# Kernel tuning notes

Measured on AMD Instinct MI355X. Metric: run time of the kernel, lower is better.

## Reference

```python
import jax, jax.numpy as jnp
import numpy as np

GROUP_SIZE = 64
SCALING = 32.0 / 16.0  # lora_alpha / r


def setup_inputs() -> dict:
    key = jax.random.key(0)
    k = jax.random.split(key, 7)
    B, S, I, O, R = 4, 2048, 4096, 4096, 16
    G = I // GROUP_SIZE
    x = jax.random.normal(k[0], (B, S, I), dtype=jnp.float32)
    W_q = jax.random.randint(k[1], (O, I), 0, 16, dtype=jnp.int32)
    scale = jax.random.uniform(k[2], (O, G), dtype=jnp.float32) * 0.01 + 1e-4
    zero = jax.random.uniform(k[3], (O, G), dtype=jnp.float32) * 8.0
    lora_A = jax.random.normal(k[4], (I, R), dtype=jnp.float32) * 0.02
    lora_B = jax.random.normal(k[5], (R, O), dtype=jnp.float32) * 0.02
    bias = jax.random.normal(k[6], (O,), dtype=jnp.float32) * 0.01
    return {"x": x, "W_q": W_q, "scale": scale, "zero": zero,
            "lora_A": lora_A, "lora_B": lora_B, "bias": bias}


def reference(x, W_q, scale, zero, lora_A, lora_B, bias):
    O, I = W_q.shape
    G = I // GROUP_SIZE
    # HQQ-style group-wise affine dequant: W = (W_q - zero) * scale  -> [O, I]
    Wg = W_q.reshape(O, G, GROUP_SIZE).astype(scale.dtype)
    W = ((Wg - zero[:, :, None]) * scale[:, :, None]).reshape(O, I)
    # base quantized linear: out = x @ W^T
    out = jnp.einsum('bsi,oi->bso', x, W)
    # LoRA low-rank update (dropout is Identity for p=0)
    out = out + (x @ lora_A @ lora_B) * SCALING
    # bias add
    out = out + bias
    return out
```

## Files before the change

### kernel.cpp

```cpp
#include <hip/hip_runtime.h>
#include <hip/hip_bf16.h>
#include <stdint.h>

#define M_DIM 8192
#define N_DIM 4096
#define K_DIM 4096

typedef __attribute__((ext_vector_type(8))) __bf16 bf16x8;
typedef __attribute__((ext_vector_type(4))) float f32x4;

__device__ inline unsigned short f2bf(float f) {
  unsigned u = __builtin_bit_cast(unsigned, f);
  u += 0x7FFF + ((u >> 16) & 1);
  return (unsigned short)(u >> 16);
}

__device__ inline void async_copy16(const void* g, void* l) {
  __builtin_amdgcn_global_load_lds(
      (const __attribute__((address_space(1))) unsigned int*)g,
      (__attribute__((address_space(3))) unsigned int*)l, 16, 0, 0);
}

__global__ __launch_bounds__(256) void cvt_x_kernel(const float* __restrict__ x,
                                                    unsigned short* __restrict__ xb,
                                                    int n4) {
  int i = blockIdx.x * 256 + threadIdx.x;
  int stride = gridDim.x * 256;
  for (; i < n4; i += stride) {
    float4 v = reinterpret_cast<const float4*>(x)[i];
    ushort4 o;
    o.x = f2bf(v.x); o.y = f2bf(v.y); o.z = f2bf(v.z); o.w = f2bf(v.w);
    reinterpret_cast<ushort4*>(xb)[i] = o;
  }
}

__global__ __launch_bounds__(256) void build_weff_kernel(
    const int* __restrict__ Wq, const float* __restrict__ scale,
    const float* __restrict__ zero, const float* __restrict__ A,
    const float* __restrict__ Bm, unsigned short* __restrict__ Weff) {
  __shared__ float sA[64 * 17];
  __shared__ float sB[16 * 64];
  int bo = blockIdx.x >> 6;
  int bi = blockIdx.x & 63;
  int o0 = bo * 64, i0 = bi * 64;
  int t = threadIdx.x;
  for (int j = t; j < 1024; j += 256) sA[(j >> 4) * 17 + (j & 15)] = A[i0 * 16 + j];
  for (int j = t; j < 1024; j += 256) sB[j] = Bm[(j >> 6) * N_DIM + o0 + (j & 63)];
  __syncthreads();
  for (int e = 0; e < 16; ++e) {
    int idx = e * 256 + t;
    int oo = idx >> 6, ii = idx & 63;
    int o = o0 + oo;
    float sc = scale[o * 64 + bi];
    float zp = zero[o * 64 + bi];
    float w = ((float)Wq[(size_t)o * K_DIM + i0 + ii] - zp) * sc;
    float acc = 0.f;
#pragma unroll
    for (int r = 0; r < 16; ++r) acc += sA[ii * 17 + r] * sB[r * 64 + oo];
    w += 2.0f * acc;
    Weff[(size_t)o * K_DIM + i0 + ii] = f2bf(w);
  }
}

#define BAR() __builtin_amdgcn_s_barrier()
#define SB()  __builtin_amdgcn_sched_barrier(0)
#define WAIT_LGKM() do { asm volatile("s_waitcnt lgkmcnt(0)" ::: "memory"); SB(); } while (0)
#define WAIT_VM4()  do { asm volatile("s_waitcnt vmcnt(4)" ::: "memory"); } while (0)

__device__ __forceinline__ bf16x8 lds_frag(const unsigned short* region, int row, int c) {
  return *reinterpret_cast<const bf16x8*>(region + row * 64 + ((c ^ (row & 7)) << 3));
}

__device__ __forceinline__ void readA(const unsigned short* reg, int mh, int lc, int lr,
                                      bf16x8 a[4][2]) {
#pragma unroll
  for (int m = 0; m < 4; ++m) {
    int row = mh * 64 + m * 16 + lc;
#pragma unroll
    for (int kk = 0; kk < 2; ++kk) a[m][kk] = lds_frag(reg, row, kk * 4 + lr);
  }
}

__device__ __forceinline__ void readB(const unsigned short* reg, int nh, int rB, int lc, int lr,
                                      bf16x8 b[2][2]) {
#pragma unroll
  for (int n = 0; n < 2; ++n) {
    int row = rB + (nh * 2 + n) * 16 + lc;
#pragma unroll
    for (int kk = 0; kk < 2; ++kk) b[n][kk] = lds_frag(reg, row, kk * 4 + lr);
  }
}

__device__ __forceinline__ void mfma_quad(const bf16x8 a[4][2], const bf16x8 b[2][2],
                                          f32x4 acc[8][4], int mh, int nh) {
  __builtin_amdgcn_s_setprio(1);
#pragma unroll
  for (int m = 0; m < 4; ++m)
#pragma unroll
    for (int n = 0; n < 2; ++n)
#pragma unroll
      for (int kk = 0; kk < 2; ++kk)
        acc[mh * 4 + m][nh * 2 + n] = __builtin_amdgcn_mfma_f32_16x16x32_bf16(
            a[m][kk], b[n][kk], acc[mh * 4 + m][nh * 2 + n], 0, 0, 0);
  __builtin_amdgcn_s_setprio(0);
}

__global__ __launch_bounds__(512, 2) void gemm_kernel(
    const unsigned short* __restrict__ xb, const unsigned short* __restrict__ wb,
    const float* __restrict__ bias, float* __restrict__ out) {
  __shared__ unsigned short lds[65536];

  int bid = blockIdx.x;
  int swz = (bid & 7) * 64 + (bid >> 3);
  int mt = swz >> 4, nt = swz & 15;
  int m0 = mt * 256, n0 = nt * 256;

  int tid = threadIdx.x;
  int w = tid >> 6, lane = tid & 63;
  int wr = w >> 2, wc = w & 3;
  int lr = lane >> 4, lc = lane & 15;

  int r0 = tid >> 3, c0g = (tid & 7) ^ (r0 & 7);
  int ch1 = 512 + tid;
  int r1 = ch1 >> 3, c1g = (ch1 & 7) ^ (r1 & 7);
  int co0 = tid * 8, co1 = ch1 * 8;

  const unsigned short* sA[2][2];
  const unsigned short* sB[2][2];
  sA[0][0] = xb + (size_t)(m0 + r0) * K_DIM + c0g * 8;
  sA[0][1] = xb + (size_t)(m0 + r1) * K_DIM + c1g * 8;
  sA[1][0] = xb + (size_t)(m0 + 128 + r0) * K_DIM + c0g * 8;
  sA[1][1] = xb + (size_t)(m0 + 128 + r1) * K_DIM + c1g * 8;
  sB[0][0] = wb + (size_t)(n0 + r0) * K_DIM + c0g * 8;
  sB[0][1] = wb + (size_t)(n0 + r1) * K_DIM + c1g * 8;
  sB[1][0] = wb + (size_t)(n0 + 128 + r0) * K_DIM + c0g * 8;
  sB[1][1] = wb + (size_t)(n0 + 128 + r1) * K_DIM + c1g * 8;

#define STAGE_A(h, buf, kt) do { \
    async_copy16(sA[h][0] + (kt), &lds[(buf) * 32768 + (h) * 8192 + co0]); \
    async_copy16(sA[h][1] + (kt), &lds[(buf) * 32768 + (h) * 8192 + co1]); } while (0)
#define STAGE_B(h, buf, kt) do { \
    async_copy16(sB[h][0] + (kt), &lds[(buf) * 32768 + 16384 + (h) * 8192 + co0]); \
    async_copy16(sB[h][1] + (kt), &lds[(buf) * 32768 + 16384 + (h) * 8192 + co1]); } while (0)

  const unsigned short* aR[2] = { &lds[wr * 8192], &lds[32768 + wr * 8192] };
  const unsigned short* bR[2] = { &lds[16384 + (wc >> 1) * 8192],
                                  &lds[32768 + 16384 + (wc >> 1) * 8192] };
  int rB = (wc & 1) * 64;

  f32x4 acc[8][4];
#pragma unroll
  for (int i = 0; i < 8; ++i)
#pragma unroll
    for (int j = 0; j < 4; ++j) acc[i][j] = f32x4{0.f, 0.f, 0.f, 0.f};

  STAGE_A(0, 0, 0); STAGE_A(1, 0, 0); STAGE_B(0, 0, 0); STAGE_B(1, 0, 0);
  STAGE_B(0, 1, 64); STAGE_A(0, 1, 64);
  WAIT_VM4(); BAR(); SB();

  bf16x8 a[4][2], b0[2][2], b1[2][2];

#pragma unroll 1
  for (int i = 0; i < 32; ++i) {
    int k1 = (2 * i + 1) * 64;
    int k2 = ((2 * i + 2) & 63) * 64;
    int k3 = ((2 * i + 3) & 63) * 64;

    readA(aR[0], 0, lc, lr, a); readB(bR[0], 0, rB, lc, lr, b0);
    STAGE_A(1, 1, k1);
    SB(); BAR(); WAIT_LGKM();
    mfma_quad(a, b0, acc, 0, 0);
    SB(); BAR(); SB();
    readB(bR[0], 1, rB, lc, lr, b1);
    STAGE_B(1, 1, k1);
    SB(); BAR(); WAIT_LGKM();
    mfma_quad(a, b1, acc, 0, 1);
    SB(); BAR(); SB();
    readA(aR[0], 1, lc, lr, a);
    STAGE_B(0, 0, k2);
    SB(); BAR(); WAIT_LGKM();
    mfma_quad(a, b1, acc, 1, 1);
    SB(); BAR(); SB();
    STAGE_A(0, 0, k2);
    SB(); BAR();
    mfma_quad(a, b0, acc, 1, 0);
    SB(); WAIT_VM4(); BAR(); SB();
    readA(aR[1], 0, lc, lr, a); readB(bR[1], 0, rB, lc, lr, b0);
    STAGE_A(1, 0, k2);
    SB(); BAR(); WAIT_LGKM();
    mfma_quad(a, b0, acc, 0, 0);
    SB(); BAR(); SB();
    readB(bR[1], 1, rB, lc, lr, b1);
    STAGE_B(1, 0, k2);
    SB(); BAR(); WAIT_LGKM();
    mfma_quad(a, b1, acc, 0, 1);
    SB(); BAR(); SB();
    readA(aR[1], 1, lc, lr, a);
    STAGE_B(0, 1, k3);
    SB(); BAR(); WAIT_LGKM();
    mfma_quad(a, b1, acc, 1, 1);
    SB(); BAR(); SB();
    STAGE_A(0, 1, k3);
    SB(); BAR();
    mfma_quad(a, b0, acc, 1, 0);
    SB(); WAIT_VM4(); BAR(); SB();
  }

#pragma unroll
  for (int ni = 0; ni < 4; ++ni) {
    int n = n0 + wc * 64 + ni * 16 + lc;
    float bv = bias[n];
#pragma unroll
    for (int mi = 0; mi < 8; ++mi) {
      int mb = m0 + wr * 128 + mi * 16 + lr * 4;
#pragma unroll
      for (int j = 0; j < 4; ++j)
        out[(size_t)(mb + j) * N_DIM + n] = acc[mi][ni][j] + bv;
    }
  }
#undef STAGE_A
#undef STAGE_B
}

extern "C" void kernel_launch(void* const* d_in, const int* in_sizes, int n_in,
                              void* d_out, int out_size, void* d_ws, size_t ws_size,
                              hipStream_t stream) {
  const float* x     = (const float*)d_in[0];
  const int*   Wq    = (const int*)d_in[1];
  const float* scale = (const float*)d_in[2];
  const float* zero  = (const float*)d_in[3];
  const float* lA    = (const float*)d_in[4];
  const float* lB    = (const float*)d_in[5];
  const float* bias  = (const float*)d_in[6];
  float* out = (float*)d_out;

  unsigned short* xb = (unsigned short*)d_ws;
  unsigned short* wb = (unsigned short*)((char*)d_ws + (size_t)M_DIM * K_DIM * 2);

  cvt_x_kernel<<<2048, 256, 0, stream>>>(x, xb, (M_DIM * K_DIM) / 4);
  build_weff_kernel<<<4096, 256, 0, stream>>>(Wq, scale, zero, lA, lB, wb);
  gemm_kernel<<<512, 512, 0, stream>>>(xb, wb, bias, out);
}
```

Before: 334.9 us.

## Switch GEMM to 32x32x16 MFMA and merge prep kernels into one launch

Replaces the 16x16x32 bf16 MFMA tiling with 32x32x16 instructions: fewer, larger MFMAs per phase, and a matching change to how fragments are read from LDS. The staging order is adjusted so both B halves are prefetched together, with the vmcnt threshold raised from 4 to 6. The x conversion and the effective-weight build are merged into a single launch that splits work by block index, which removes one kernel launch. The larger MFMA should cut LDS fragment traffic per flop, at the cost of a different epilogue layout and altered prefetch timing.

```diff
diff --git a/kernel.cpp b/kernel.cpp
--- a/kernel.cpp
+++ b/kernel.cpp
@@ -7,7 +7,7 @@
 #define K_DIM 4096
 
 typedef __attribute__((ext_vector_type(8))) __bf16 bf16x8;
-typedef __attribute__((ext_vector_type(4))) float f32x4;
+typedef __attribute__((ext_vector_type(16))) float f32x16;
 
 __device__ inline unsigned short f2bf(float f) {
   unsigned u = __builtin_bit_cast(unsigned, f);
@@ -21,87 +21,84 @@
       (__attribute__((address_space(3))) unsigned int*)l, 16, 0, 0);
 }
 
-__global__ __launch_bounds__(256) void cvt_x_kernel(const float* __restrict__ x,
-                                                    unsigned short* __restrict__ xb,
-                                                    int n4) {
-  int i = blockIdx.x * 256 + threadIdx.x;
-  int stride = gridDim.x * 256;
-  for (; i < n4; i += stride) {
-    float4 v = reinterpret_cast<const float4*>(x)[i];
-    ushort4 o;
-    o.x = f2bf(v.x); o.y = f2bf(v.y); o.z = f2bf(v.z); o.w = f2bf(v.w);
-    reinterpret_cast<ushort4*>(xb)[i] = o;
-  }
-}
-
-__global__ __launch_bounds__(256) void build_weff_kernel(
+__global__ __launch_bounds__(256) void prep_kernel(
+    const float* __restrict__ x, unsigned short* __restrict__ xb,
     const int* __restrict__ Wq, const float* __restrict__ scale,
     const float* __restrict__ zero, const float* __restrict__ A,
     const float* __restrict__ Bm, unsigned short* __restrict__ Weff) {
-  __shared__ float sA[64 * 17];
-  __shared__ float sB[16 * 64];
-  int bo = blockIdx.x >> 6;
-  int bi = blockIdx.x & 63;
-  int o0 = bo * 64, i0 = bi * 64;
   int t = threadIdx.x;
-  for (int j = t; j < 1024; j += 256) sA[(j >> 4) * 17 + (j & 15)] = A[i0 * 16 + j];
-  for (int j = t; j < 1024; j += 256) sB[j] = Bm[(j >> 6) * N_DIM + o0 + (j & 63)];
-  __syncthreads();
-  for (int e = 0; e < 16; ++e) {
-    int idx = e * 256 + t;
-    int oo = idx >> 6, ii = idx & 63;
-    int o = o0 + oo;
-    float sc = scale[o * 64 + bi];
-    float zp = zero[o * 64 + bi];
-    float w = ((float)Wq[(size_t)o * K_DIM + i0 + ii] - zp) * sc;
-    float acc = 0.f;
-#pragma unroll
-    for (int r = 0; r < 16; ++r) acc += sA[ii * 17 + r] * sB[r * 64 + oo];
-    w += 2.0f * acc;
-    Weff[(size_t)o * K_DIM + i0 + ii] = f2bf(w);
+  if (blockIdx.x < 4096) {
+    __shared__ float sA[64 * 17];
+    __shared__ float sB[16 * 64];
+    int bo = blockIdx.x >> 6;
+    int bi = blockIdx.x & 63;
+    int o0 = bo * 64, i0 = bi * 64;
+    for (int j = t; j < 1024; j += 256) sA[(j >> 4) * 17 + (j & 15)] = A[i0 * 16 + j];
+    for (int j = t; j < 1024; j += 256) sB[j] = Bm[(j >> 6) * N_DIM + o0 + (j & 63)];
+    __syncthreads();
+    for (int e = 0; e < 16; ++e) {
+      int idx = e * 256 + t;
+      int oo = idx >> 6, ii = idx & 63;
+      int o = o0 + oo;
+      float sc = scale[o * 64 + bi];
+      float zp = zero[o * 64 + bi];
+      float w = ((float)Wq[(size_t)o * K_DIM + i0 + ii] - zp) * sc;
+      float acc = 0.f;
+#pragma unroll
+      for (int r = 0; r < 16; ++r) acc += sA[ii * 17 + r] * sB[r * 64 + oo];
+      w += 2.0f * acc;
+      Weff[(size_t)o * K_DIM + i0 + ii] = f2bf(w);
+    }
+  } else {
+    int i = (blockIdx.x - 4096) * 256 + t;
+    int stride = 2048 * 256;
+    int n4 = (M_DIM * K_DIM) / 4;
+    for (; i < n4; i += stride) {
+      float4 v = reinterpret_cast<const float4*>(x)[i];
+      ushort4 o;
+      o.x = f2bf(v.x); o.y = f2bf(v.y); o.z = f2bf(v.z); o.w = f2bf(v.w);
+      reinterpret_cast<ushort4*>(xb)[i] = o;
+    }
   }
 }
 
 #define BAR() __builtin_amdgcn_s_barrier()
 #define SB()  __builtin_amdgcn_sched_barrier(0)
 #define WAIT_LGKM() do { asm volatile("s_waitcnt lgkmcnt(0)" ::: "memory"); SB(); } while (0)
-#define WAIT_VM4()  do { asm volatile("s_waitcnt vmcnt(4)" ::: "memory"); } while (0)
+#define WAIT_VM6()  do { asm volatile("s_waitcnt vmcnt(6)" ::: "memory"); } while (0)
 
 __device__ __forceinline__ bf16x8 lds_frag(const unsigned short* region, int row, int c) {
   return *reinterpret_cast<const bf16x8*>(region + row * 64 + ((c ^ (row & 7)) << 3));
 }
 
-__device__ __forceinline__ void readA(const unsigned short* reg, int mh, int lc, int lr,
-                                      bf16x8 a[4][2]) {
-#pragma unroll
-  for (int m = 0; m < 4; ++m) {
-    int row = mh * 64 + m * 16 + lc;
-#pragma unroll
-    for (int kk = 0; kk < 2; ++kk) a[m][kk] = lds_frag(reg, row, kk * 4 + lr);
-  }
-}
-
-__device__ __forceinline__ void readB(const unsigned short* reg, int nh, int rB, int lc, int lr,
-                                      bf16x8 b[2][2]) {
-#pragma unroll
-  for (int n = 0; n < 2; ++n) {
-    int row = rB + (nh * 2 + n) * 16 + lc;
-#pragma unroll
-    for (int kk = 0; kk < 2; ++kk) b[n][kk] = lds_frag(reg, row, kk * 4 + lr);
-  }
-}
-
-__device__ __forceinline__ void mfma_quad(const bf16x8 a[4][2], const bf16x8 b[2][2],
-                                          f32x4 acc[8][4], int mh, int nh) {
+__device__ __forceinline__ void readA32(const unsigned short* reg, int mh, int lane,
+                                        bf16x8 a[2][4]) {
+  int r = lane & 31, hi = lane >> 5;
+#pragma unroll
+  for (int rt = 0; rt < 2; ++rt) {
+    int row = mh * 64 + rt * 32 + r;
+#pragma unroll
+    for (int ks = 0; ks < 4; ++ks) a[rt][ks] = lds_frag(reg, row, ks * 2 + hi);
+  }
+}
+
+__device__ __forceinline__ void readB32(const unsigned short* reg, int rB, int nh, int lane,
+                                        bf16x8 b[4]) {
+  int r = lane & 31, hi = lane >> 5;
+  int row = rB + nh * 32 + r;
+#pragma unroll
+  for (int ks = 0; ks < 4; ++ks) b[ks] = lds_frag(reg, row, ks * 2 + hi);
+}
+
+__device__ __forceinline__ void mfma_phase32(const bf16x8 a[2][4], const bf16x8 b[4],
+                                             f32x16 acc[4][2], int mh, int nh) {
   __builtin_amdgcn_s_setprio(1);
 #pragma unroll
-  for (int m = 0; m < 4; ++m)
-#pragma unroll
-    for (int n = 0; n < 2; ++n)
-#pragma unroll
-      for (int kk = 0; kk < 2; ++kk)
-        acc[mh * 4 + m][nh * 2 + n] = __builtin_amdgcn_mfma_f32_16x16x32_bf16(
-            a[m][kk], b[n][kk], acc[mh * 4 + m][nh * 2 + n], 0, 0, 0);
+  for (int ks = 0; ks < 4; ++ks)
+#pragma unroll
+    for (int rt = 0; rt < 2; ++rt)
+      acc[mh * 2 + rt][nh] = __builtin_amdgcn_mfma_f32_32x32x16_bf16(
+          a[rt][ks], b[ks], acc[mh * 2 + rt][nh], 0, 0, 0);
   __builtin_amdgcn_s_setprio(0);
 }
 
@@ -118,7 +115,7 @@
   int tid = threadIdx.x;
   int w = tid >> 6, lane = tid & 63;
   int wr = w >> 2, wc = w & 3;
-  int lr = lane >> 4, lc = lane & 15;
+  int rB = (wc & 1) * 64;
 
   int r0 = tid >> 3, c0g = (tid & 7) ^ (r0 & 7);
   int ch1 = 512 + tid;
@@ -146,19 +143,18 @@
   const unsigned short* aR[2] = { &lds[wr * 8192], &lds[32768 + wr * 8192] };
   const unsigned short* bR[2] = { &lds[16384 + (wc >> 1) * 8192],
                                   &lds[32768 + 16384 + (wc >> 1) * 8192] };
-  int rB = (wc & 1) * 64;
-
-  f32x4 acc[8][4];
-#pragma unroll
-  for (int i = 0; i < 8; ++i)
-#pragma unroll
-    for (int j = 0; j < 4; ++j) acc[i][j] = f32x4{0.f, 0.f, 0.f, 0.f};
-
-  STAGE_A(0, 0, 0); STAGE_A(1, 0, 0); STAGE_B(0, 0, 0); STAGE_B(1, 0, 0);
-  STAGE_B(0, 1, 64); STAGE_A(0, 1, 64);
-  WAIT_VM4(); BAR(); SB();
-
-  bf16x8 a[4][2], b0[2][2], b1[2][2];
+
+  f32x16 acc[4][2];
+#pragma unroll
+  for (int i = 0; i < 4; ++i)
+#pragma unroll
+    for (int j = 0; j < 2; ++j) acc[i][j] = (f32x16)(0.f);
+
+  STAGE_A(0, 0, 0); STAGE_B(0, 0, 0); STAGE_B(1, 0, 0); STAGE_A(1, 0, 0);
+  STAGE_B(0, 1, 64); STAGE_B(1, 1, 64); STAGE_A(0, 1, 64);
+  WAIT_VM6(); BAR(); SB();
+
+  bf16x8 a[2][4], b0[4], b1[4];
 
 #pragma unroll 1
   for (int i = 0; i < 32; ++i) {
@@ -166,56 +162,58 @@
     int k2 = ((2 * i + 2) & 63) * 64;
     int k3 = ((2 * i + 3) & 63) * 64;
 
-    readA(aR[0], 0, lc, lr, a); readB(bR[0], 0, rB, lc, lr, b0);
+    readA32(aR[0], 0, lane, a); readB32(bR[0], rB, 0, lane, b0);
     STAGE_A(1, 1, k1);
     SB(); BAR(); WAIT_LGKM();
-    mfma_quad(a, b0, acc, 0, 0);
-    SB(); BAR(); SB();
-    readB(bR[0], 1, rB, lc, lr, b1);
-    STAGE_B(1, 1, k1);
-    SB(); BAR(); WAIT_LGKM();
-    mfma_quad(a, b1, acc, 0, 1);
-    SB(); BAR(); SB();
-    readA(aR[0], 1, lc, lr, a);
+    mfma_phase32(a, b0, acc, 0, 0);
+    SB(); BAR(); SB();
+    readB32(bR[0], rB, 1, lane, b1);
+    SB(); BAR(); WAIT_LGKM();
+    mfma_phase32(a, b1, acc, 0, 1);
+    SB(); BAR(); SB();
+    readA32(aR[0], 1, lane, a);
     STAGE_B(0, 0, k2);
     SB(); BAR(); WAIT_LGKM();
-    mfma_quad(a, b1, acc, 1, 1);
-    SB(); BAR(); SB();
-    STAGE_A(0, 0, k2);
+    mfma_phase32(a, b1, acc, 1, 1);
+    SB(); BAR(); SB();
+    STAGE_B(1, 0, k2); STAGE_A(0, 0, k2);
     SB(); BAR();
-    mfma_quad(a, b0, acc, 1, 0);
-    SB(); WAIT_VM4(); BAR(); SB();
-    readA(aR[1], 0, lc, lr, a); readB(bR[1], 0, rB, lc, lr, b0);
+    mfma_phase32(a, b0, acc, 1, 0);
+    SB(); WAIT_VM6(); BAR(); SB();
+    readA32(aR[1], 0, lane, a); readB32(bR[1], rB, 0, lane, b0);
     STAGE_A(1, 0, k2);
     SB(); BAR(); WAIT_LGKM();
-    mfma_quad(a, b0, acc, 0, 0);
-    SB(); BAR(); SB();
-    readB(bR[1], 1, rB, lc, lr, b1);
-    STAGE_B(1, 0, k2);
-    SB(); BAR(); WAIT_LGKM();
-    mfma_quad(a, b1, acc, 0, 1);
-    SB(); BAR(); SB();
-    readA(aR[1], 1, lc, lr, a);
+    mfma_phase32(a, b0, acc, 0, 0);
+    SB(); BAR(); SB();
+    readB32(bR[1], rB, 1, lane, b1);
+    SB(); BAR(); WAIT_LGKM();
+    mfma_phase32(a, b1, acc, 0, 1);
+    SB(); BAR(); SB();
+    readA32(aR[1], 1, lane, a);
     STAGE_B(0, 1, k3);
     SB(); BAR(); WAIT_LGKM();
-    mfma_quad(a, b1, acc, 1, 1);
-    SB(); BAR(); SB();
-    STAGE_A(0, 1, k3);
+    mfma_phase32(a, b1, acc, 1, 1);
+    SB(); BAR(); SB();
+    STAGE_B(1, 1, k3); STAGE_A(0, 1, k3);
     SB(); BAR();
-    mfma_quad(a, b0, acc, 1, 0);
-    SB(); WAIT_VM4(); BAR(); SB();
-  }
-
-#pragma unroll
-  for (int ni = 0; ni < 4; ++ni) {
-    int n = n0 + wc * 64 + ni * 16 + lc;
+    mfma_phase32(a, b0, acc, 1, 0);
+    SB(); WAIT_VM6(); BAR(); SB();
+  }
+  asm volatile("s_waitcnt vmcnt(0)" ::: "memory");
+
+  int col = lane & 31, hi = lane >> 5;
+#pragma unroll
+  for (int ni = 0; ni < 2; ++ni) {
+    int n = n0 + wc * 64 + ni * 32 + col;
     float bv = bias[n];
 #pragma unroll
-    for (int mi = 0; mi < 8; ++mi) {
-      int mb = m0 + wr * 128 + mi * 16 + lr * 4;
-#pragma unroll
-      for (int j = 0; j < 4; ++j)
-        out[(size_t)(mb + j) * N_DIM + n] = acc[mi][ni][j] + bv;
+    for (int mi = 0; mi < 4; ++mi) {
+      int mbase = m0 + wr * 128 + mi * 32 + 4 * hi;
+#pragma unroll
+      for (int r = 0; r < 16; ++r) {
+        int m = mbase + (r & 3) + 8 * (r >> 2);
+        out[(size_t)m * N_DIM + n] = acc[mi][ni][r] + bv;
+      }
     }
   }
 #undef STAGE_A
@@ -237,7 +235,6 @@
   unsigned short* xb = (unsigned short*)d_ws;
   unsigned short* wb = (unsigned short*)((char*)d_ws + (size_t)M_DIM * K_DIM * 2);
 
-  cvt_x_kernel<<<2048, 256, 0, stream>>>(x, xb, (M_DIM * K_DIM) / 4);
-  build_weff_kernel<<<4096, 256, 0, stream>>>(Wq, scale, zero, lA, lB, wb);
+  prep_kernel<<<6144, 256, 0, stream>>>(x, xb, Wq, scale, zero, lA, lB, wb);
   gemm_kernel<<<512, 512, 0, stream>>>(xb, wb, bias, out);
 }
```

New measurement: 350.2 us. 1.05x slower.

## Merge prep kernels into one launch and prefetch B half-tiles earlier in GEMM

Applied to the files above, without the earlier changes.

The x-to-bf16 conversion and the effective-weight build now run as one kernel, with blocks split by index, which removes a launch and lets the two memory-bound jobs overlap. In the GEMM main loop, the second B half-tile for the next stage is issued earlier, next to the A half-tile prefetch, and the wait threshold goes from vmcnt(4) to vmcnt(6) to match. This gives B loads more time to arrive before they are used. A final vmcnt(0) drains outstanding loads before the epilogue, and more loads are in flight at each point.

```diff
diff --git a/kernel.cpp b/kernel.cpp
--- a/kernel.cpp
+++ b/kernel.cpp
@@ -21,51 +21,51 @@
       (__attribute__((address_space(3))) unsigned int*)l, 16, 0, 0);
 }
 
-__global__ __launch_bounds__(256) void cvt_x_kernel(const float* __restrict__ x,
-                                                    unsigned short* __restrict__ xb,
-                                                    int n4) {
-  int i = blockIdx.x * 256 + threadIdx.x;
-  int stride = gridDim.x * 256;
-  for (; i < n4; i += stride) {
-    float4 v = reinterpret_cast<const float4*>(x)[i];
-    ushort4 o;
-    o.x = f2bf(v.x); o.y = f2bf(v.y); o.z = f2bf(v.z); o.w = f2bf(v.w);
-    reinterpret_cast<ushort4*>(xb)[i] = o;
-  }
-}
-
-__global__ __launch_bounds__(256) void build_weff_kernel(
+__global__ __launch_bounds__(256) void prep_kernel(
+    const float* __restrict__ x, unsigned short* __restrict__ xb,
     const int* __restrict__ Wq, const float* __restrict__ scale,
     const float* __restrict__ zero, const float* __restrict__ A,
     const float* __restrict__ Bm, unsigned short* __restrict__ Weff) {
-  __shared__ float sA[64 * 17];
-  __shared__ float sB[16 * 64];
-  int bo = blockIdx.x >> 6;
-  int bi = blockIdx.x & 63;
-  int o0 = bo * 64, i0 = bi * 64;
   int t = threadIdx.x;
-  for (int j = t; j < 1024; j += 256) sA[(j >> 4) * 17 + (j & 15)] = A[i0 * 16 + j];
-  for (int j = t; j < 1024; j += 256) sB[j] = Bm[(j >> 6) * N_DIM + o0 + (j & 63)];
-  __syncthreads();
-  for (int e = 0; e < 16; ++e) {
-    int idx = e * 256 + t;
-    int oo = idx >> 6, ii = idx & 63;
-    int o = o0 + oo;
-    float sc = scale[o * 64 + bi];
-    float zp = zero[o * 64 + bi];
-    float w = ((float)Wq[(size_t)o * K_DIM + i0 + ii] - zp) * sc;
-    float acc = 0.f;
-#pragma unroll
-    for (int r = 0; r < 16; ++r) acc += sA[ii * 17 + r] * sB[r * 64 + oo];
-    w += 2.0f * acc;
-    Weff[(size_t)o * K_DIM + i0 + ii] = f2bf(w);
+  if (blockIdx.x < 4096) {
+    __shared__ float sA[64 * 17];
+    __shared__ float sB[16 * 64];
+    int bo = blockIdx.x >> 6;
+    int bi = blockIdx.x & 63;
+    int o0 = bo * 64, i0 = bi * 64;
+    for (int j = t; j < 1024; j += 256) sA[(j >> 4) * 17 + (j & 15)] = A[i0 * 16 + j];
+    for (int j = t; j < 1024; j += 256) sB[j] = Bm[(j >> 6) * N_DIM + o0 + (j & 63)];
+    __syncthreads();
+    for (int e = 0; e < 16; ++e) {
+      int idx = e * 256 + t;
+      int oo = idx >> 6, ii = idx & 63;
+      int o = o0 + oo;
+      float sc = scale[o * 64 + bi];
+      float zp = zero[o * 64 + bi];
+      float w = ((float)Wq[(size_t)o * K_DIM + i0 + ii] - zp) * sc;
+      float acc = 0.f;
+#pragma unroll
+      for (int r = 0; r < 16; ++r) acc += sA[ii * 17 + r] * sB[r * 64 + oo];
+      w += 2.0f * acc;
+      Weff[(size_t)o * K_DIM + i0 + ii] = f2bf(w);
+    }
+  } else {
+    int i = (blockIdx.x - 4096) * 256 + t;
+    int stride = 2048 * 256;
+    int n4 = (M_DIM * K_DIM) / 4;
+    for (; i < n4; i += stride) {
+      float4 v = reinterpret_cast<const float4*>(x)[i];
+      ushort4 o;
+      o.x = f2bf(v.x); o.y = f2bf(v.y); o.z = f2bf(v.z); o.w = f2bf(v.w);
+      reinterpret_cast<ushort4*>(xb)[i] = o;
+    }
   }
 }
 
 #define BAR() __builtin_amdgcn_s_barrier()
 #define SB()  __builtin_amdgcn_sched_barrier(0)
 #define WAIT_LGKM() do { asm volatile("s_waitcnt lgkmcnt(0)" ::: "memory"); SB(); } while (0)
-#define WAIT_VM4()  do { asm volatile("s_waitcnt vmcnt(4)" ::: "memory"); } while (0)
+#define WAIT_VM6()  do { asm volatile("s_waitcnt vmcnt(6)" ::: "memory"); } while (0)
 
 __device__ __forceinline__ bf16x8 lds_frag(const unsigned short* region, int row, int c) {
   return *reinterpret_cast<const bf16x8*>(region + row * 64 + ((c ^ (row & 7)) << 3));
@@ -119,6 +119,7 @@
   int w = tid >> 6, lane = tid & 63;
   int wr = w >> 2, wc = w & 3;
   int lr = lane >> 4, lc = lane & 15;
+  int rB = (wc & 1) * 64;
 
   int r0 = tid >> 3, c0g = (tid & 7) ^ (r0 & 7);
   int ch1 = 512 + tid;
@@ -146,7 +147,6 @@
   const unsigned short* aR[2] = { &lds[wr * 8192], &lds[32768 + wr * 8192] };
   const unsigned short* bR[2] = { &lds[16384 + (wc >> 1) * 8192],
                                   &lds[32768 + 16384 + (wc >> 1) * 8192] };
-  int rB = (wc & 1) * 64;
 
   f32x4 acc[8][4];
 #pragma unroll
@@ -154,9 +154,9 @@
 #pragma unroll
     for (int j = 0; j < 4; ++j) acc[i][j] = f32x4{0.f, 0.f, 0.f, 0.f};
 
-  STAGE_A(0, 0, 0); STAGE_A(1, 0, 0); STAGE_B(0, 0, 0); STAGE_B(1, 0, 0);
-  STAGE_B(0, 1, 64); STAGE_A(0, 1, 64);
-  WAIT_VM4(); BAR(); SB();
+  STAGE_A(0, 0, 0); STAGE_B(0, 0, 0); STAGE_B(1, 0, 0); STAGE_A(1, 0, 0);
+  STAGE_B(0, 1, 64); STAGE_B(1, 1, 64); STAGE_A(0, 1, 64);
+  WAIT_VM6(); BAR(); SB();
 
   bf16x8 a[4][2], b0[2][2], b1[2][2];
 
@@ -172,7 +172,6 @@
     mfma_quad(a, b0, acc, 0, 0);
     SB(); BAR(); SB();
     readB(bR[0], 1, rB, lc, lr, b1);
-    STAGE_B(1, 1, k1);
     SB(); BAR(); WAIT_LGKM();
     mfma_quad(a, b1, acc, 0, 1);
     SB(); BAR(); SB();
@@ -181,17 +180,16 @@
     SB(); BAR(); WAIT_LGKM();
     mfma_quad(a, b1, acc, 1, 1);
     SB(); BAR(); SB();
-    STAGE_A(0, 0, k2);
+    STAGE_B(1, 0, k2); STAGE_A(0, 0, k2);
     SB(); BAR();
     mfma_quad(a, b0, acc, 1, 0);
-    SB(); WAIT_VM4(); BAR(); SB();
+    SB(); WAIT_VM6(); BAR(); SB();
     readA(aR[1], 0, lc, lr, a); readB(bR[1], 0, rB, lc, lr, b0);
     STAGE_A(1, 0, k2);
     SB(); BAR(); WAIT_LGKM();
     mfma_quad(a, b0, acc, 0, 0);
     SB(); BAR(); SB();
     readB(bR[1], 1, rB, lc, lr, b1);
-    STAGE_B(1, 0, k2);
     SB(); BAR(); WAIT_LGKM();
     mfma_quad(a, b1, acc, 0, 1);
     SB(); BAR(); SB();
@@ -200,11 +198,12 @@
     SB(); BAR(); WAIT_LGKM();
     mfma_quad(a, b1, acc, 1, 1);
     SB(); BAR(); SB();
-    STAGE_A(0, 1, k3);
+    STAGE_B(1, 1, k3); STAGE_A(0, 1, k3);
     SB(); BAR();
     mfma_quad(a, b0, acc, 1, 0);
-    SB(); WAIT_VM4(); BAR(); SB();
-  }
+    SB(); WAIT_VM6(); BAR(); SB();
+  }
+  asm volatile("s_waitcnt vmcnt(0)" ::: "memory");
 
 #pragma unroll
   for (int ni = 0; ni < 4; ++ni) {
@@ -237,7 +236,6 @@
   unsigned short* xb = (unsigned short*)d_ws;
   unsigned short* wb = (unsigned short*)((char*)d_ws + (size_t)M_DIM * K_DIM * 2);
 
-  cvt_x_kernel<<<2048, 256, 0, stream>>>(x, xb, (M_DIM * K_DIM) / 4);
-  build_weff_kernel<<<4096, 256, 0, stream>>>(Wq, scale, zero, lA, lB, wb);
+  prep_kernel<<<6144, 256, 0, stream>>>(x, xb, Wq, scale, zero, lA, lB, wb);
   gemm_kernel<<<512, 512, 0, stream>>>(xb, wb, bias, out);
 }
```

After: 319.8 us. 1.05x faster.
